# Kernel optimization log

Hardware: AMD Instinct MI355X
Metric: run time of the kernel (lower is better)

## Reference

```python
import jax, jax.numpy as jnp
import numpy as np

D_MODEL = 1024
N_HEADS = 16
D_K = D_MODEL // N_HEADS


def setup_inputs() -> dict:
    key = jax.random.key(0)
    ks = jax.random.split(key, 9)
    s = 1.0 / np.sqrt(D_MODEL)
    return {
        "x": jax.random.normal(ks[0], (4, 2048, D_MODEL), dtype=jnp.float32),
        "Wq": jax.random.normal(ks[1], (D_MODEL, D_MODEL), dtype=jnp.float32) * s,
        "bq": jax.random.normal(ks[2], (D_MODEL,), dtype=jnp.float32) * 0.01,
        "Wk": jax.random.normal(ks[3], (D_MODEL, D_MODEL), dtype=jnp.float32) * s,
        "bk": jax.random.normal(ks[4], (D_MODEL,), dtype=jnp.float32) * 0.01,
        "Wv": jax.random.normal(ks[5], (D_MODEL, D_MODEL), dtype=jnp.float32) * s,
        "bv": jax.random.normal(ks[6], (D_MODEL,), dtype=jnp.float32) * 0.01,
        "Wo": jax.random.normal(ks[7], (D_MODEL, D_MODEL), dtype=jnp.float32) * s,
        "bo": jax.random.normal(ks[8], (D_MODEL,), dtype=jnp.float32) * 0.01,
    }


def reference(x, Wq, bq, Wk, bk, Wv, bv, Wo, bo):
    B, S, _ = x.shape
    # projections (torch Linear: x @ W.T + b; here W stored as [in, out])
    q = (x @ Wq + bq).reshape(B, S, N_HEADS, D_K).transpose(0, 2, 1, 3)  # [B,H,S,Dk]
    k = (x @ Wk + bk).reshape(B, S, N_HEADS, D_K).transpose(0, 2, 1, 3)
    v = (x @ Wv + bv).reshape(B, S, N_HEADS, D_K).transpose(0, 2, 1, 3)
    scale = 1.0 / np.sqrt(D_K).astype(np.float32)
    scores = jnp.einsum("bhsd,bhtd->bhst", q, k) * scale  # [B,H,S,S]
    attn = jax.nn.softmax(scores, axis=-1)
    ctx = jnp.einsum("bhst,bhtd->bhsd", attn, v)  # [B,H,S,Dk]
    ctx = ctx.transpose(0, 2, 1, 3).reshape(B, S, D_MODEL)
    return ctx @ Wo + bo
```

## Files before the change

### kernel.cpp

```cpp
#include <hip/hip_runtime.h>
#include <math.h>

#define DMODEL 1024
#define NHEADS 16
#define DKDIM  64
#define SEQLEN 2048
#define NBATCH 4
#define MTOT   (NBATCH * SEQLEN)


typedef __attribute__((ext_vector_type(8)))  short short8;
typedef __attribute__((ext_vector_type(4)))  float f32x4;
typedef __attribute__((ext_vector_type(16))) float f32x16;

__device__ __forceinline__ unsigned short f2bf(float x) {
    unsigned u = __builtin_bit_cast(unsigned, x);
    unsigned r = (u + 0x7fffu + ((u >> 16) & 1u)) >> 16;
    return (unsigned short)r;
}

__device__ __forceinline__ void gload16(const void* g, void* l) {
    __builtin_amdgcn_global_load_lds(
        (const __attribute__((address_space(1))) void*)g,
        (__attribute__((address_space(3))) void*)l, 16, 0, 0);
}

__global__ __launch_bounds__(256)
void convert_x_kernel(const float* __restrict__ x, unsigned short* __restrict__ xb)
{
    const size_t i = ((size_t)blockIdx.x * 256 + threadIdx.x) * 8;
    const float4 a = *(const float4*)&x[i];
    const float4 b = *(const float4*)&x[i + 4];
    union { unsigned short u[8]; uint4 q; } p;
    p.u[0] = f2bf(a.x); p.u[1] = f2bf(a.y); p.u[2] = f2bf(a.z); p.u[3] = f2bf(a.w);
    p.u[4] = f2bf(b.x); p.u[5] = f2bf(b.y); p.u[6] = f2bf(b.z); p.u[7] = f2bf(b.w);
    *(uint4*)&xb[i] = p.q;
}

__global__ __launch_bounds__(256)
void convert_w_kernel(const float* __restrict__ W0, const float* __restrict__ W1,
                      const float* __restrict__ W2, const float* __restrict__ W3,
                      unsigned short* __restrict__ wt)
{
    const int z = blockIdx.z;
    const float* W = (z == 0) ? W0 : (z == 1) ? W1 : (z == 2) ? W2 : W3;
    unsigned short* dst = wt + (size_t)z * DMODEL * DMODEL;
    const int n0 = blockIdx.x * 64, k0 = blockIdx.y * 64;
    __shared__ float T[64][65];
    const int t = threadIdx.x;
    const int r0 = t >> 4, c0 = (t & 15) << 2;
#pragma unroll
    for (int u = 0; u < 4; ++u) {
        const float4 wv = *(const float4*)&W[(size_t)(k0 + r0 + u * 16) * DMODEL + n0 + c0];
        T[c0 + 0][r0 + u * 16] = wv.x;
        T[c0 + 1][r0 + u * 16] = wv.y;
        T[c0 + 2][r0 + u * 16] = wv.z;
        T[c0 + 3][r0 + u * 16] = wv.w;
    }
    __syncthreads();
    const int rn = t >> 2, ck = (t & 3) << 4;
    union { unsigned short u16[16]; uint4 q[2]; } pk;
#pragma unroll
    for (int e = 0; e < 16; ++e) pk.u16[e] = f2bf(T[rn][ck + e]);
    *(uint4*)&dst[(size_t)(n0 + rn) * DMODEL + k0 + ck]     = pk.q[0];
    *(uint4*)&dst[(size_t)(n0 + rn) * DMODEL + k0 + ck + 8] = pk.q[1];
}

template<int OMODE>
__device__ __forceinline__
void gemm_core(const unsigned short* __restrict__ A, const unsigned short* __restrict__ Bt,
               const float* __restrict__ bias, void* __restrict__ outv, const float scl)
{
    __shared__ __align__(16) char As[128 * 128];
    __shared__ __align__(16) char Bs[128 * 128];

    const int t  = threadIdx.x;
    const int l  = t & 63, w = t >> 6;
    const int g  = (l >> 4), lr = l & 15;
    const int wr = w >> 1, wc = w & 1;
    const int swz = (lr & 7) << 4;

    const int flat = (blockIdx.y << 3) | blockIdx.x;
    const int sid  = ((flat & 7) << 6) | (flat >> 3);
    const int m0 = (sid >> 3) << 7;
    const int n0 = (sid & 7) << 7;

    f32x4 acc[4][4];
#pragma unroll
    for (int i = 0; i < 4; ++i)
#pragma unroll
        for (int j = 0; j < 4; ++j) acc[i][j] = (f32x4){0.f, 0.f, 0.f, 0.f};

    for (int k0 = 0; k0 < DMODEL; k0 += 64) {
        __syncthreads();
#pragma unroll
        for (int qd = 0; qd < 4; ++qd) {
            const int o   = (t + qd * 256) << 4;
            const int row = o >> 7;
            const int c   = (o & 127) ^ ((row & 7) << 4);
            gload16((const char*)A  + (((size_t)(m0 + row) * DMODEL + k0) << 1) + c, As + o);
            gload16((const char*)Bt + (((size_t)(n0 + row) * DMODEL + k0) << 1) + c, Bs + o);
        }
        __syncthreads();

        short8 af[4][2], bf[4][2];
#pragma unroll
        for (int i = 0; i < 4; ++i)
#pragma unroll
            for (int kk = 0; kk < 2; ++kk) {
                const int off = (kk * 64 + g * 16) ^ swz;
                af[i][kk] = *(const short8*)(As + (wr * 64 + i * 16 + lr) * 128 + off);
                bf[i][kk] = *(const short8*)(Bs + (wc * 64 + i * 16 + lr) * 128 + off);
            }
        __builtin_amdgcn_s_setprio(1);
#pragma unroll
        for (int kk = 0; kk < 2; ++kk)
#pragma unroll
            for (int i = 0; i < 4; ++i)
#pragma unroll
                for (int j = 0; j < 4; ++j)
                    acc[i][j] = __builtin_amdgcn_mfma_f32_16x16x32_bf16(
                        af[i][kk], bf[j][kk], acc[i][j], 0, 0, 0);
        __builtin_amdgcn_s_setprio(0);
    }

    float bj[4];
#pragma unroll
    for (int j = 0; j < 4; ++j) bj[j] = bias[n0 + wc * 64 + j * 16 + lr];

#pragma unroll
    for (int i = 0; i < 4; ++i)
#pragma unroll
        for (int j = 0; j < 4; ++j) {
            const int mb = m0 + wr * 64 + i * 16 + g * 4;
            const int n  = n0 + wc * 64 + j * 16 + lr;
            float v[4];
#pragma unroll
            for (int r = 0; r < 4; ++r) v[r] = (acc[i][j][r] + bj[j]) * scl;
            if (OMODE == 0) {
                unsigned short* outp = (unsigned short*)outv;
#pragma unroll
                for (int r = 0; r < 4; ++r)
                    outp[(size_t)(mb + r) * DMODEL + n] = f2bf(v[r]);
            } else if (OMODE == 1) {
                unsigned short* outp = (unsigned short*)outv;
                const int b = mb >> 11, s = mb & (SEQLEN - 1);
                const size_t idx = (((size_t)(b * NHEADS + (n >> 6)) * DKDIM + (n & 63)) << 11) + s;
                uint2 pk;
                pk.x = (unsigned)f2bf(v[0]) | ((unsigned)f2bf(v[1]) << 16);
                pk.y = (unsigned)f2bf(v[2]) | ((unsigned)f2bf(v[3]) << 16);
                *(uint2*)&outp[idx] = pk;
            } else {
                float* outp = (float*)outv;
#pragma unroll
                for (int r = 0; r < 4; ++r)
                    outp[(size_t)(mb + r) * DMODEL + n] = v[r];
            }
        }
}

#define QSCALE 0.1803368801111137f

__global__ __launch_bounds__(256)
void qkv_gemm_kernel(const unsigned short* __restrict__ xb, const unsigned short* __restrict__ wt,
                     const float* __restrict__ bq, const float* __restrict__ bk,
                     const float* __restrict__ bv,
                     unsigned short* __restrict__ Qb, unsigned short* __restrict__ Kb,
                     unsigned short* __restrict__ Vt)
{
    if (blockIdx.z == 0)      gemm_core<0>(xb, wt,                      bq, Qb, QSCALE);
    else if (blockIdx.z == 1) gemm_core<0>(xb, wt + DMODEL * DMODEL,     bk, Kb, 1.0f);
    else                      gemm_core<1>(xb, wt + 2 * DMODEL * DMODEL, bv, Vt, 1.0f);
}

__global__ __launch_bounds__(256)
void out_gemm_kernel(const unsigned short* __restrict__ ctx, const unsigned short* __restrict__ wt,
                     const float* __restrict__ bo, float* __restrict__ out)
{
    gemm_core<2>(ctx, wt + 3 * DMODEL * DMODEL, bo, out, 1.0f);
}

__device__ __forceinline__
void attn_body(const char* __restrict__ Kbuf, const char* __restrict__ Vbuf,
               const short8 (&qf)[4], const short8 ones, const f32x16& z16,
               f32x16 (&po)[2], f32x16& po_l,
               int q32, int hi, int swz)
{
#pragma unroll
    for (int hf = 0; hf < 2; ++hf) {
        short8 kf[4];
#pragma unroll
        for (int kk = 0; kk < 4; ++kk)
            kf[kk] = *(const short8*)(Kbuf + (hf * 32 + q32) * 128 + ((kk * 32 + hi * 16) ^ swz));
        __builtin_amdgcn_s_setprio(1);
        f32x16 s = __builtin_amdgcn_mfma_f32_32x32x16_bf16(kf[0], qf[0], z16, 0, 0, 0);
#pragma unroll
        for (int kk = 1; kk < 4; ++kk)
            s = __builtin_amdgcn_mfma_f32_32x32x16_bf16(kf[kk], qf[kk], s, 0, 0, 0);
        __builtin_amdgcn_s_setprio(0);

#pragma unroll
        for (int r = 0; r < 16; ++r) s[r] = __builtin_amdgcn_exp2f(s[r]);

        short8 pf[2];
#pragma unroll
        for (int j = 0; j < 2; ++j) {
            const int bse = j * 8;
            unsigned wA0, wA1, wB0, wB1;
            asm("v_cvt_pk_bf16_f32 %0, %1, %2" : "=v"(wA0) : "v"(s[bse + 0]), "v"(s[bse + 1]));
            asm("v_cvt_pk_bf16_f32 %0, %1, %2" : "=v"(wA1) : "v"(s[bse + 2]), "v"(s[bse + 3]));
            asm("v_cvt_pk_bf16_f32 %0, %1, %2" : "=v"(wB0) : "v"(s[bse + 4]), "v"(s[bse + 5]));
            asm("v_cvt_pk_bf16_f32 %0, %1, %2" : "=v"(wB1) : "v"(s[bse + 6]), "v"(s[bse + 7]));
            asm volatile("v_permlane32_swap_b32 %0, %1" : "+v"(wA0), "+v"(wB0));
            asm volatile("v_permlane32_swap_b32 %0, %1" : "+v"(wA1), "+v"(wB1));
            union { unsigned u[4]; short8 s8; } pk;
            pk.u[0] = wA0; pk.u[1] = wA1; pk.u[2] = wB0; pk.u[3] = wB1;
            pf[j] = pk.s8;
        }

        short8 vf0[2], vf1[2];
#pragma unroll
        for (int j = 0; j < 2; ++j) {
            const int ks = hf * 2 + j;
            vf0[j] = *(const short8*)(Vbuf + q32 * 128 + ((ks * 32 + hi * 16) ^ swz));
            vf1[j] = *(const short8*)(Vbuf + (32 + q32) * 128 + ((ks * 32 + hi * 16) ^ swz));
        }
        __builtin_amdgcn_s_setprio(1);
#pragma unroll
        for (int j = 0; j < 2; ++j) {
            po[0] = __builtin_amdgcn_mfma_f32_32x32x16_bf16(vf0[j], pf[j], po[0], 0, 0, 0);
            po[1] = __builtin_amdgcn_mfma_f32_32x32x16_bf16(vf1[j], pf[j], po[1], 0, 0, 0);
            po_l  = __builtin_amdgcn_mfma_f32_32x32x16_bf16(ones,   pf[j], po_l,  0, 0, 0);
        }
        __builtin_amdgcn_s_setprio(0);
    }
}

__global__ __launch_bounds__(512)
void attn_kernel(const unsigned short* __restrict__ Qb, const unsigned short* __restrict__ Kb,
                 const unsigned short* __restrict__ Vt, unsigned short* __restrict__ ctx)
{
    __shared__ __align__(16) char smem[49152];

    const int t   = threadIdx.x;
    const int l   = t & 63, w = t >> 6;
    const int q32 = l & 31, hi = l >> 5;
    const int swz = (q32 & 7) << 4;

    const int flat = (blockIdx.y << 3) | blockIdx.x;
    const int sid  = ((flat & 7) << 6) | (flat >> 3);
    const int qt = sid & 7;
    const int bh = sid >> 3;
    const int b  = bh >> 4, h = bh & 15;
    const int coln = h * DKDIM;

    const size_t qrow  = (size_t)b * SEQLEN + qt * 256 + w * 32 + q32;
    const size_t krow0 = (size_t)b * SEQLEN;
    const size_t vbase = (size_t)(b * NHEADS + h) * DKDIM * SEQLEN;

    short8 qf[4];
#pragma unroll
    for (int kk = 0; kk < 4; ++kk)
        qf[kk] = *(const short8*)(Qb + qrow * DMODEL + coln + kk * 16 + hi * 8);

    short8 ones;
#pragma unroll
    for (int e = 0; e < 8; ++e) ones[e] = (short)0x3F80;

    f32x16 z16;
#pragma unroll
    for (int r = 0; r < 16; ++r) z16[r] = 0.f;

    f32x16 po[2], po_l;
#pragma unroll
    for (int r = 0; r < 16; ++r) { po[0][r] = 0.f; po[1][r] = 0.f; po_l[r] = 0.f; }

    const int so   = t << 4;
    const int srow = so >> 7;
    const int sc_  = (so & 127) ^ ((srow & 7) << 4);

#define STAGE(bufidx, kt)                                                                    \
    do {                                                                                     \
        gload16((const char*)Kb + (((krow0 + (kt) * 64 + srow) * DMODEL + coln) << 1) + sc_, \
                smem + (bufidx) * 8192 + so);                                                \
        gload16((const char*)Vt + ((vbase + (size_t)srow * SEQLEN + (kt) * 64) << 1) + sc_,  \
                smem + 24576 + (bufidx) * 8192 + so);                                        \
    } while (0)
#define BODY(bufidx)                                                            \
    attn_body(smem + (bufidx) * 8192, smem + 24576 + (bufidx) * 8192,           \
              qf, ones, z16, po, po_l, q32, hi, swz)

    STAGE(0, 0);
    STAGE(1, 1);

#pragma unroll 1
    for (int kt = 0; kt < 30; kt += 3) {
        asm volatile("s_waitcnt vmcnt(2)" ::: "memory");
        __builtin_amdgcn_s_barrier();
        STAGE(2, kt + 2);
        BODY(0);

        asm volatile("s_waitcnt vmcnt(2)" ::: "memory");
        __builtin_amdgcn_s_barrier();
        STAGE(0, kt + 3);
        BODY(1);

        asm volatile("s_waitcnt vmcnt(2)" ::: "memory");
        __builtin_amdgcn_s_barrier();
        STAGE(1, kt + 4);
        BODY(2);
    }

    asm volatile("s_waitcnt vmcnt(2)" ::: "memory");
    __builtin_amdgcn_s_barrier();
    BODY(0);
    asm volatile("s_waitcnt vmcnt(0)" ::: "memory");
    __builtin_amdgcn_s_barrier();
    BODY(1);

    __syncthreads();

    const float inv = 1.0f / po_l[0];
    char* T = smem + w * 4096;
#pragma unroll
    for (int i = 0; i < 2; ++i)
#pragma unroll
        for (int g4 = 0; g4 < 4; ++g4) {
            const int d0 = i * 32 + g4 * 8 + hi * 4;
            uint2 pk;
            pk.x = (unsigned)f2bf(po[i][g4 * 4 + 0] * inv) | ((unsigned)f2bf(po[i][g4 * 4 + 1] * inv) << 16);
            pk.y = (unsigned)f2bf(po[i][g4 * 4 + 2] * inv) | ((unsigned)f2bf(po[i][g4 * 4 + 3] * inv) << 16);
            *(uint2*)(T + ((q32 * 128 + d0 * 2) ^ swz)) = pk;
        }
    __syncthreads();
#pragma unroll
    for (int pass = 0; pass < 4; ++pass) {
        const int o   = (l + pass * 64) << 4;
        const int row = o >> 7;
        const int c   = o & 127;
        const uint4 val = *(const uint4*)(T + (o ^ ((row & 7) << 4)));
        const size_t token = (size_t)b * SEQLEN + qt * 256 + w * 32 + row;
        *(uint4*)&ctx[token * DMODEL + coln + (c >> 1)] = val;
    }
#undef STAGE
#undef BODY
}

extern "C" void kernel_launch(void* const* d_in, const int* in_sizes, int n_in,
                              void* d_out, int out_size, void* d_ws, size_t ws_size,
                              hipStream_t stream)
{
    const float* x  = (const float*)d_in[0];
    const float* Wq = (const float*)d_in[1];
    const float* bq = (const float*)d_in[2];
    const float* Wk = (const float*)d_in[3];
    const float* bk = (const float*)d_in[4];
    const float* Wv = (const float*)d_in[5];
    const float* bv = (const float*)d_in[6];
    const float* Wo = (const float*)d_in[7];
    const float* bo = (const float*)d_in[8];
    float* out = (float*)d_out;

    const size_t NE = (size_t)MTOT * DMODEL;
    unsigned short* xb  = (unsigned short*)d_ws;
    unsigned short* wt  = xb  + NE;
    unsigned short* Qb  = wt  + (size_t)4 * DMODEL * DMODEL;
    unsigned short* Kb  = Qb  + NE;
    unsigned short* Vt  = Kb  + NE;
    unsigned short* ctx = Vt  + NE;

    convert_x_kernel<<<dim3(NE / (256 * 8)), 256, 0, stream>>>(x, xb);
    convert_w_kernel<<<dim3(16, 16, 4), 256, 0, stream>>>(Wq, Wk, Wv, Wo, wt);
    qkv_gemm_kernel<<<dim3(8, 64, 3), 256, 0, stream>>>(xb, wt, bq, bk, bv, Qb, Kb, Vt);
    attn_kernel<<<dim3(SEQLEN / 256, NBATCH * NHEADS), dim3(512), 0, stream>>>(Qb, Kb, Vt, ctx);
    out_gemm_kernel<<<dim3(8, 64), 256, 0, stream>>>(ctx, wt, bo, out);
}
```

Measured before the change: 176.8 us.

## Double-buffer 128-key attention tiles and merge conversion kernels into one launch

The attention kernel moves from a triple-buffered 64-key pipeline with vmcnt waits to a double-buffered 128-key pipeline using full __syncthreads. Each stage now loads 128 keys, and the body processes four 32-key halves, so the loop does half as many barriers. Shared memory grows to 64 KB per block, which may lower occupancy, and the coarser waits may expose load latency. The x and W fp32-to-bf16 conversion kernels are also merged into a single launch to save launch overhead.

After: 175.8 us. Within noise of the previous version (-0.6%).

```diff
diff --git a/kernel.cpp b/kernel.cpp
--- a/kernel.cpp
+++ b/kernel.cpp
@@ -26,28 +26,29 @@
 }
 
 __global__ __launch_bounds__(256)
-void convert_x_kernel(const float* __restrict__ x, unsigned short* __restrict__ xb)
-{
-    const size_t i = ((size_t)blockIdx.x * 256 + threadIdx.x) * 8;
-    const float4 a = *(const float4*)&x[i];
-    const float4 b = *(const float4*)&x[i + 4];
-    union { unsigned short u[8]; uint4 q; } p;
-    p.u[0] = f2bf(a.x); p.u[1] = f2bf(a.y); p.u[2] = f2bf(a.z); p.u[3] = f2bf(a.w);
-    p.u[4] = f2bf(b.x); p.u[5] = f2bf(b.y); p.u[6] = f2bf(b.z); p.u[7] = f2bf(b.w);
-    *(uint4*)&xb[i] = p.q;
-}
-
-__global__ __launch_bounds__(256)
-void convert_w_kernel(const float* __restrict__ W0, const float* __restrict__ W1,
-                      const float* __restrict__ W2, const float* __restrict__ W3,
-                      unsigned short* __restrict__ wt)
-{
-    const int z = blockIdx.z;
+void convert_all_kernel(const float* __restrict__ x,
+                        const float* __restrict__ W0, const float* __restrict__ W1,
+                        const float* __restrict__ W2, const float* __restrict__ W3,
+                        unsigned short* __restrict__ xb, unsigned short* __restrict__ wt)
+{
+    const int bid = blockIdx.x;
+    const int t = threadIdx.x;
+    if (bid < 4096) {
+        const size_t i = ((size_t)bid * 256 + t) * 8;
+        const float4 a = *(const float4*)&x[i];
+        const float4 b = *(const float4*)&x[i + 4];
+        union { unsigned short u[8]; uint4 q; } p;
+        p.u[0] = f2bf(a.x); p.u[1] = f2bf(a.y); p.u[2] = f2bf(a.z); p.u[3] = f2bf(a.w);
+        p.u[4] = f2bf(b.x); p.u[5] = f2bf(b.y); p.u[6] = f2bf(b.z); p.u[7] = f2bf(b.w);
+        *(uint4*)&xb[i] = p.q;
+        return;
+    }
+    const int wid = bid - 4096;
+    const int z  = wid >> 8;
     const float* W = (z == 0) ? W0 : (z == 1) ? W1 : (z == 2) ? W2 : W3;
     unsigned short* dst = wt + (size_t)z * DMODEL * DMODEL;
-    const int n0 = blockIdx.x * 64, k0 = blockIdx.y * 64;
+    const int n0 = ((wid >> 4) & 15) * 64, k0 = (wid & 15) * 64;
     __shared__ float T[64][65];
-    const int t = threadIdx.x;
     const int r0 = t >> 4, c0 = (t & 15) << 2;
 #pragma unroll
     for (int u = 0; u < 4; ++u) {
@@ -181,13 +182,13 @@
 }
 
 __device__ __forceinline__
-void attn_body(const char* __restrict__ Kbuf, const char* __restrict__ Vbuf,
-               const short8 (&qf)[4], const short8 ones, const f32x16& z16,
-               f32x16 (&po)[2], f32x16& po_l,
-               int q32, int hi, int swz)
-{
-#pragma unroll
-    for (int hf = 0; hf < 2; ++hf) {
+void attn_body4(const char* __restrict__ Kbuf, const char* __restrict__ Vbuf,
+                const short8 (&qf)[4], const short8 ones, const f32x16& z16,
+                f32x16 (&po)[2], f32x16& po_l,
+                int q32, int hi, int swz)
+{
+#pragma unroll
+    for (int hf = 0; hf < 4; ++hf) {
         short8 kf[4];
 #pragma unroll
         for (int kk = 0; kk < 4; ++kk)
@@ -222,8 +223,8 @@
 #pragma unroll
         for (int j = 0; j < 2; ++j) {
             const int ks = hf * 2 + j;
-            vf0[j] = *(const short8*)(Vbuf + q32 * 128 + ((ks * 32 + hi * 16) ^ swz));
-            vf1[j] = *(const short8*)(Vbuf + (32 + q32) * 128 + ((ks * 32 + hi * 16) ^ swz));
+            vf0[j] = *(const short8*)(Vbuf + q32 * 256 + ((ks * 32 + hi * 16) ^ swz));
+            vf1[j] = *(const short8*)(Vbuf + (32 + q32) * 256 + ((ks * 32 + hi * 16) ^ swz));
         }
         __builtin_amdgcn_s_setprio(1);
 #pragma unroll
@@ -240,7 +241,7 @@
 void attn_kernel(const unsigned short* __restrict__ Qb, const unsigned short* __restrict__ Kb,
                  const unsigned short* __restrict__ Vt, unsigned short* __restrict__ ctx)
 {
-    __shared__ __align__(16) char smem[49152];
+    __shared__ __align__(16) char smem[65536];
 
     const int t   = threadIdx.x;
     const int l   = t & 63, w = t >> 6;
@@ -276,46 +277,42 @@
     for (int r = 0; r < 16; ++r) { po[0][r] = 0.f; po[1][r] = 0.f; po_l[r] = 0.f; }
 
     const int so   = t << 4;
-    const int srow = so >> 7;
-    const int sc_  = (so & 127) ^ ((srow & 7) << 4);
-
-#define STAGE(bufidx, kt)                                                                    \
-    do {                                                                                     \
-        gload16((const char*)Kb + (((krow0 + (kt) * 64 + srow) * DMODEL + coln) << 1) + sc_, \
-                smem + (bufidx) * 8192 + so);                                                \
-        gload16((const char*)Vt + ((vbase + (size_t)srow * SEQLEN + (kt) * 64) << 1) + sc_,  \
-                smem + 24576 + (bufidx) * 8192 + so);                                        \
+    const int kr   = so >> 7;
+    const int ksc  = (so & 127) ^ ((kr & 7) << 4);
+    const int vr   = so >> 8;
+    const int vsc  = (so & 255) ^ ((vr & 7) << 4);
+
+#define KBUF(i) (smem + (i) * 16384)
+#define VBUF(i) (smem + 32768 + (i) * 16384)
+#define STAGE(bufidx, kt)                                                                         \
+    do {                                                                                          \
+        gload16((const char*)Kb + (((krow0 + (kt) * 128 + kr)      * DMODEL + coln) << 1) + ksc,  \
+                KBUF(bufidx) + so);                                                               \
+        gload16((const char*)Kb + (((krow0 + (kt) * 128 + kr + 64) * DMODEL + coln) << 1) + ksc,  \
+                KBUF(bufidx) + so + 8192);                                                        \
+        gload16((const char*)Vt + ((vbase + (size_t)vr        * SEQLEN + (kt) * 128) << 1) + vsc, \
+                VBUF(bufidx) + so);                                                               \
+        gload16((const char*)Vt + ((vbase + (size_t)(vr + 32) * SEQLEN + (kt) * 128) << 1) + vsc, \
+                VBUF(bufidx) + so + 8192);                                                        \
     } while (0)
 #define BODY(bufidx)                                                            \
-    attn_body(smem + (bufidx) * 8192, smem + 24576 + (bufidx) * 8192,           \
-              qf, ones, z16, po, po_l, q32, hi, swz)
+    attn_body4(KBUF(bufidx), VBUF(bufidx), qf, ones, z16, po, po_l, q32, hi, swz)
 
     STAGE(0, 0);
-    STAGE(1, 1);
+    __syncthreads();
 
 #pragma unroll 1
-    for (int kt = 0; kt < 30; kt += 3) {
-        asm volatile("s_waitcnt vmcnt(2)" ::: "memory");
-        __builtin_amdgcn_s_barrier();
-        STAGE(2, kt + 2);
+    for (int kt = 0; kt < 14; kt += 2) {
+        STAGE(1, kt + 1);
         BODY(0);
-
-        asm volatile("s_waitcnt vmcnt(2)" ::: "memory");
-        __builtin_amdgcn_s_barrier();
-        STAGE(0, kt + 3);
+        __syncthreads();
+        STAGE(0, kt + 2);
         BODY(1);
-
-        asm volatile("s_waitcnt vmcnt(2)" ::: "memory");
-        __builtin_amdgcn_s_barrier();
-        STAGE(1, kt + 4);
-        BODY(2);
-    }
-
-    asm volatile("s_waitcnt vmcnt(2)" ::: "memory");
-    __builtin_amdgcn_s_barrier();
+        __syncthreads();
+    }
+    STAGE(1, 15);
     BODY(0);
-    asm volatile("s_waitcnt vmcnt(0)" ::: "memory");
-    __builtin_amdgcn_s_barrier();
+    __syncthreads();
     BODY(1);
 
     __syncthreads();
@@ -344,6 +341,8 @@
     }
 #undef STAGE
 #undef BODY
+#undef KBUF
+#undef VBUF
 }
 
 extern "C" void kernel_launch(void* const* d_in, const int* in_sizes, int n_in,
@@ -369,8 +368,7 @@
     unsigned short* Vt  = Kb  + NE;
     unsigned short* ctx = Vt  + NE;
 
-    convert_x_kernel<<<dim3(NE / (256 * 8)), 256, 0, stream>>>(x, xb);
-    convert_w_kernel<<<dim3(16, 16, 4), 256, 0, stream>>>(Wq, Wk, Wv, Wo, wt);
+    convert_all_kernel<<<dim3(4096 + 1024), 256, 0, stream>>>(x, Wq, Wk, Wv, Wo, xb, wt);
     qkv_gemm_kernel<<<dim3(8, 64, 3), 256, 0, stream>>>(xb, wt, bq, bk, bv, Qb, Kb, Vt);
     attn_kernel<<<dim3(SEQLEN / 256, NBATCH * NHEADS), dim3(512), 0, stream>>>(Qb, Kb, Vt, ctx);
     out_gemm_kernel<<<dim3(8, 64), 256, 0, stream>>>(ctx, wt, bo, out);
```
